# Kernel optimization log

Measured on AMD Instinct MI355X. Metric: run time of the kernel, lower is better.

Reference implementation:

```python
import jax, jax.numpy as jnp
import numpy as np

EPS = 1e-8
CG_TOL = 1e-4
S_SIGMA = 8   # bilateral grid spatial downsampling
N_BINS = 9    # bilateral grid range bins (intensity in [0,1])


def _conv2d(x, k):
    # x [C,H,W], k [kh,kw] -> same-padded cross-correlation, per channel
    kh, kw = k.shape
    out = jax.lax.conv_general_dilated(x[:, None], k[None, None], (1, 1),
                                       [(kh // 2, kh // 2), (kw // 2, kw // 2)])
    return out[:, 0]


def _conv2d_T(x, k):
    return _conv2d(x, k[::-1, ::-1])


def _conv_bank(x, ks):
    # x [C,H,W], ks [N,kh,kw] -> [N,C,H,W]
    n, kh, kw = ks.shape
    out = jax.lax.conv_general_dilated(x[:, None], ks[:, None], (1, 1),
                                       [(kh // 2, kh // 2), (kw // 2, kw // 2)])
    return out.transpose(1, 0, 2, 3)


def _conv_bank_T(v, ks):
    # v [N,C,H,W] -> sum_n conv(v[n], flip(ks[n])) : [C,H,W]
    n, kh, kw = ks.shape
    lhs = v.transpose(1, 0, 2, 3)          # [C,N,H,W]
    rhs = ks[:, ::-1, ::-1][None]          # [1,N,kh,kw]
    out = jax.lax.conv_general_dilated(lhs, rhs, (1, 1),
                                       [(kh // 2, kh // 2), (kw // 2, kw // 2)])
    return out[:, 0]


def _deconv_grad(blurred, x, kernel, dkw, dks, rkw, rks, rpow, reg_targets):
    # gradient of E(x) = sum_i dkw_i ||dk_i * (k*x - b)||^2
    #                  + sum_j rkw_j sum |rk_j*x - t_j|^{p_j}
    Kx = _conv2d(x, kernel) - blurred
    d = _conv_bank(Kx, dks)                                    # [Nd,C,H,W]
    g = _conv2d_T(_conv_bank_T(2.0 * dkw[:, None, None, None] * d, dks), kernel)
    v = _conv_bank(x, rks) - reg_targets                       # [Nr,C,H,W]
    av = jnp.abs(v) + EPS
    phi = jnp.sign(v) * av ** (rpow[:, None, None, None] - 1.0)
    g = g + _conv_bank_T(rkw[:, None, None, None] * rpow[:, None, None, None] * phi, rks)
    return g


def _deconv_alpha(blurred, x, kernel, dkw, dks, rkw, rks, rpow, reg_targets, p):
    # exact line search for the quadratic part, Gauss-Newton for |.|^p prior
    g = _deconv_grad(blurred, x, kernel, dkw, dks, rkw, rks, rpow, reg_targets)
    num = -jnp.sum(g * p)
    Kp = _conv2d(p, kernel)
    dKp = _conv_bank(Kp, dks)
    den = jnp.sum(2.0 * dkw[:, None, None, None] * dKp ** 2)
    v = _conv_bank(x, rks) - reg_targets
    Rp = _conv_bank(p, rks)
    w = (rkw * rpow * (rpow - 1.0))[:, None, None, None]
    den = den + jnp.sum(w * (jnp.abs(v) + EPS) ** (rpow[:, None, None, None] - 2.0) * Rp ** 2)
    return num / (den + 1e-12)


def _deconv_prior(x, rks, thr):
    # soft-shrinkage of filtered responses -> regularization targets
    v = _conv_bank(x, rks)
    return jnp.sign(v) * jnp.maximum(jnp.abs(v) - thr[:, None, None, None], 0.0)


def _conv_axis(g, f, axis):
    k = f.shape[0]; r = k // 2; L = g.shape[axis]
    pad = [(0, 0)] * g.ndim; pad[axis] = (r, r)
    gp = jnp.pad(g, pad)
    out = jnp.zeros_like(g)
    for t in range(k):  # fixed small tap count
        out = out + f[t] * jax.lax.slice_in_dim(gp, t, t + L, axis=axis)
    return out


def _bilateral_channel(I, fs, fr):
    # learned-filter bilateral grid: splat -> separable filter (fs,fs,fr) -> trilinear slice
    H, W = I.shape
    gh, gw = H // S_SIGMA, W // S_SIGMA
    Ic = jnp.clip(I, 0.0, 1.0)
    yy, xx = jnp.meshgrid(jnp.arange(H), jnp.arange(W), indexing="ij")
    yi = yy // S_SIGMA; xi = xx // S_SIGMA
    zi = jnp.clip(jnp.round(Ic * (N_BINS - 1)).astype(jnp.int32), 0, N_BINS - 1)
    flat = ((yi * gw + xi) * N_BINS + zi).ravel()
    gv = jnp.zeros(gh * gw * N_BINS, Ic.dtype).at[flat].add(Ic.ravel())
    gw_ = jnp.zeros(gh * gw * N_BINS, Ic.dtype).at[flat].add(1.0)
    g2 = jnp.stack([gv, gw_], -1).reshape(gh, gw, N_BINS, 2)
    g2 = _conv_axis(_conv_axis(_conv_axis(g2, fs, 0), fs, 1), fr, 2)
    yf = yy / S_SIGMA; xf = xx / S_SIGMA; zf = Ic * (N_BINS - 1)

    def corners(f, n):
        c0 = jnp.clip(jnp.floor(f).astype(jnp.int32), 0, n - 1)
        c1 = jnp.minimum(c0 + 1, n - 1)
        w = jnp.clip(f - c0, 0.0, 1.0)
        return c0, c1, w

    y0, y1, wy = corners(yf, gh)
    x0, x1, wx = corners(xf, gw)
    z0, z1, wz = corners(zf, N_BINS)
    acc = jnp.zeros(I.shape + (2,), Ic.dtype)
    for yc, wyc in ((y0, 1 - wy), (y1, wy)):
        for xc, wxc in ((x0, 1 - wx), (x1, wx)):
            for zc, wzc in ((z0, 1 - wz), (z1, wz)):
                acc = acc + (wyc * wxc * wzc)[..., None] * g2[yc, xc, zc]
    return acc[..., 0] / (acc[..., 1] + 1e-8)


def _forward(blurred_batch, kernel_batch, data_kernels, data_kernel_weights,
             reg_kernels, reg_kernel_weights, reg_powers, filter_s, filter_r,
             reg_thresholds, num_cg_iter):
    num_stages = filter_s.shape[0]
    n_reg = reg_kernels.shape[1]

    def single(blurred, kernel):
        def cg(x, idx, reg_targets):
            dkw = data_kernel_weights[idx]; dks = data_kernels[idx]
            rkw = reg_kernel_weights[idx]; rks = reg_kernels[idx]; rp = reg_powers[idx]
            g = _deconv_grad(blurred, x, kernel, dkw, dks, rkw, rks, rp, reg_targets)
            r = -g
            r_norm = jnp.sum(r * r)
            r0 = r_norm

            def body(i, carry):
                x, r, p, rn, done = carry
                alpha = _deconv_alpha(blurred, x, kernel, dkw, dks, rkw, rks, rp, reg_targets, p)
                x1 = x + alpha * p
                g1 = _deconv_grad(blurred, x1, kernel, dkw, dks, rkw, rks, rp, reg_targets)
                r1 = -g1
                nrn = jnp.sum(r1 * r1)
                beta = nrn / (rn + 1e-20)
                conv_now = nrn < CG_TOL * r0
                p1 = r1 + beta * p
                x_n = jnp.where(done, x, x1)
                r_n = jnp.where(done, r, r1)
                rn_n = jnp.where(done, rn, nrn)
                p_n = jnp.where(done | conv_now, p, p1)
                return (x_n, r_n, p_n, rn_n, done | conv_now)

            carry = (x, r, r, r_norm, jnp.array(False))
            x, _, _, _, _ = jax.lax.fori_loop(0, num_cg_iter, body, carry)
            return x

        x = cg(blurred, 0, jnp.zeros((n_reg,) + blurred.shape, blurred.dtype))
        for stage in range(num_stages):
            x = jax.vmap(lambda ch: _bilateral_channel(ch, filter_s[stage], filter_r[stage]))(x)
            reg_targets = _deconv_prior(x, reg_kernels[stage + 1], reg_thresholds[stage])
            x = cg(x, stage + 1, reg_targets)
        return x

    return jax.vmap(single)(blurred_batch, kernel_batch)


def setup_inputs() -> dict:
    key = jax.random.key(0)
    k1, k2 = jax.random.split(key)
    B, C, H, W, KS = 2, 3, 512, 512, 15
    blurred = jax.random.uniform(k1, (B, C, H, W), jnp.float32)
    kern = jax.random.uniform(k2, (B, KS, KS), jnp.float32)
    kern = kern / jnp.sum(kern, axis=(1, 2), keepdims=True)  # normalized PSFs

    ns = 1; c = 2  # num_stages, kernel center (5x5)
    rk = np.zeros((ns + 1, 5, 5, 5), np.float32)
    rk[:, 0, c, c] = -1.0; rk[:, 0, c + 1, c] = 1.0
    rk[:, 1, c, c] = -1.0; rk[:, 1, c, c + 1] = 1.0
    rk[:, 2, c, c] = 1.0; rk[:, 2, c + 1, c] = -1.0
    rk[:, 2, c, c + 1] = -1.0; rk[:, 2, c + 1, c + 1] = 1.0
    rk[:, 3, c - 1, c] = 1.0; rk[:, 3, c, c] = -2.0; rk[:, 3, c + 1, c] = 1.0
    rk[:, 4, c, c - 1] = 1.0; rk[:, 4, c, c] = -2.0; rk[:, 4, c, c + 1] = 1.0
    dk = np.zeros((ns + 1, 6, 5, 5), np.float32)
    dk[:, 0, c, c] = 1.0
    dk[:, 1:] = rk
    dkw = np.zeros((ns + 1, 6), np.float32); dkw[:, 0] = 1.0
    rkw = np.zeros((ns + 1, 5), np.float32)
    rkw[0, :] = 0.001; rkw[1:, :] = 0.05
    rpow = np.full((ns + 1, 5), 2.0, np.float32)
    fs = np.zeros((ns, 11), np.float32); fs[:, 3:8] = [0.0, 1.0, 2.0, 1.0, 0.0]
    fr = np.tile(np.array([0.0, 1.0, 2.0, 1.0, 0.0], np.float32), (ns, 1))
    thr = np.tile(np.array([0.065, 0.065, 0.0325, 0.0325, 0.0325], np.float32), (ns, 1))

    return {
        "blurred_batch": blurred,
        "kernel_batch": kern,
        "data_kernels": jnp.asarray(dk),
        "data_kernel_weights": jnp.asarray(dkw),
        "reg_kernels": jnp.asarray(rk),
        "reg_kernel_weights": jnp.asarray(rkw),
        "reg_powers": jnp.asarray(rpow),
        "filter_s": jnp.asarray(fs),
        "filter_r": jnp.asarray(fr),
        "reg_thresholds": jnp.asarray(thr),
        "num_cg_iter": 5,
    }


def reference(blurred_batch, kernel_batch, data_kernels, data_kernel_weights,
              reg_kernels, reg_kernel_weights, reg_powers, filter_s, filter_r,
              reg_thresholds, num_cg_iter):
    return _forward(blurred_batch, kernel_batch, data_kernels, data_kernel_weights,
                    reg_kernels, reg_kernel_weights, reg_powers, filter_s, filter_r,
                    reg_thresholds, num_cg_iter)
```

## Files before the change

kernel.cpp:

```cpp
#include <hip/hip_runtime.h>

constexpr int Bn = 2, Cn = 3, Hh = 512, Ww = 512;
constexpr int KS = 15, KR = 7;
constexpr int NDK = 6, NRK = 5;
constexpr int GH = 64, GW = 64, NBn = 9, SS = 8;
constexpr float EPSf = 1e-8f;
constexpr float CGTOL = 1e-4f;
constexpr int PLANE = Hh * Ww;
constexpr int CHW = Cn * PLANE;
constexpr int BX = 64, BY = 16;
constexpr int GXc = Ww / BX, GYc = Hh / BY;
constexpr int PB = GXc * GYc * Cn;
constexpr int SA = 80, THt = 30;
constexpr int S2W = 72, S2H = 24;
constexpr int PHW = 68, PHH = 20;
constexpr int PHG = (PHW / 4) * PHH;
constexpr int NITER = 5;

struct CgState { float alpha, beta, rn, r0; int done, pflag; int pad0, pad1; };

struct SolveInfo {
    int fastBank;
    int allrp2;
    int nd;
    int pad;
    float sctot;
    float dsc[NDK];
    int ddy[NDK], ddx[NDK];
    float C[81];
};

__device__ __forceinline__ float blockReduce(float v, float* red, int tid) {
    red[tid] = v; __syncthreads();
    for (int s = 128; s > 0; s >>= 1) { if (tid < s) red[tid] += red[tid + s]; __syncthreads(); }
    float r = red[0]; __syncthreads();
    return r;
}

__global__ __launch_bounds__(128)
void k_comp(const float* __restrict__ dkw, const float* __restrict__ dks,
            const float* __restrict__ rkw, const float* __restrict__ rpw,
            const float* __restrict__ rks, SolveInfo* si)
{
    const int idx = blockIdx.x;
    SolveInfo* s = si + idx;
    const float* dkw_i = dkw + idx * NDK;
    const float* dks_i = dks + (size_t)idx * NDK * 25;
    const float* rkw_i = rkw + idx * NRK;
    const float* rpw_i = rpw + idx * NRK;
    const float* rks_i = rks + (size_t)idx * NRK * 25;
    const int t = threadIdx.x;
    if (t < 81) {
        int oy = t / 9 - 4, ox = t % 9 - 4;
        float acc = 0.f;
        for (int m = 0; m < NRK; m++) {
            float wm = rkw_i[m], rp = rpw_i[m];
            float ch = wm * rp * (rp - 1.f);
            if (ch == 0.f) continue;
            for (int ay = 0; ay < 5; ay++)
                for (int ax = 0; ax < 5; ax++) {
                    int by = ay - oy, bx = ax - ox;
// ... 11 lines not shown
            for (int q = 0; q < 25; q++) if (dks_i[n * 25 + q] != 0.f) { cntz++; pos = q; }
            if (cntz > 1) fast = 0;
            if (cntz == 1 && nd < NDK) {
                float v = dks_i[n * 25 + pos];
                s->dsc[nd] = 2.f * dkw_i[n] * v * v;
                s->ddy[nd] = pos / 5 - 2; s->ddx[nd] = pos % 5 - 2;
                tot += s->dsc[nd]; nd++;
            }
        }
        s->fastBank = fast; s->nd = fast ? nd : 0; s->sctot = tot;
    }
    if (t == 82) {
        int ok = 1;
        for (int m = 0; m < NRK; m++) {
            float wm = rkw_i[m], rp = rpw_i[m];
            if (wm != 0.f && rp != 2.f && wm * rp * (rp - 1.f) != 0.f) ok = 0;
        }
        s->allrp2 = ok;
    }
}

__global__ __launch_bounds__(256)
void k_conv15(const float* __restrict__ src, const float* __restrict__ rb,
              const float* __restrict__ pbuf, float* __restrict__ aux2,
              const float* __restrict__ sub, float* __restrict__ out,
              const float* __restrict__ kernB, float* __restrict__ part,
              const SolveInfo* __restrict__ si,
              const CgState* __restrict__ st, const int* __restrict__ ncg,
              int iter, int mode)
{
    const int pz = blockIdx.z, b = pz / Cn, c = pz % Cn;
    const CgState s = st[b];
    if (mode == 2 && (s.done != 0 || iter >= *ncg)) return;
    __shared__ __align__(16) float tile[SA * THt];
    __shared__ float red[256];
    const int tx = threadIdx.x, ty = threadIdx.y, tid = ty * 16 + tx;
    const int ox0 = blockIdx.x * BX, oy0 = blockIdx.y * BY;
    const int baseP = pz * PLANE;
    const float beta = s.beta; const int pf = s.pflag;
    const float* kp = kernB + b * 225;

    float nm = 0.f;
    for (int i = tid; i < 78 * THt; i += 256) {
        int ly = i / 78, lx = i % 78;
        int gy = oy0 - KR + ly, gx = ox0 - KR + lx;
        float v = 0.f;
        if (gy >= 0 && gy < Hh && gx >= 0 && gx < Ww) {
            int gi = baseP + gy * Ww + gx;
            if (mode == 2) {
                float rv = rb[gi], pv = pbuf[gi];
                v = pf ? fmaf(beta, pv, rv) : pv;
                if (ly >= KR && ly < KR + BY && lx >= KR && lx < KR + BX) {
                    nm = fmaf(rv, v, nm);
                    aux2[gi] = v;
                }
            } else {
                v = src[gi];
                if (mode == 0 && ly >= KR && ly < KR + BY && lx >= KR && lx < KR + BX)
                    aux2[gi] = v;
            }
        }
        tile[ly * SA + lx] = v;
    }
    __syncthreads();

    const int colbase = tx * 4;
    float a0 = 0.f, a1 = 0.f, a2 = 0.f, a3 = 0.f;
    for (int i = 0; i < KS; i++) {
        const float4* rp4 = reinterpret_cast<const float4*>(&tile[(ty + i) * SA + colbase]);
        float f[20];
        #pragma unroll
        for (int s5 = 0; s5 < 5; s5++) {
            float4 w4 = rp4[s5];
            f[s5 * 4] = w4.x; f[s5 * 4 + 1] = w4.y; f[s5 * 4 + 2] = w4.z; f[s5 * 4 + 3] = w4.w;
        }
        const float* kr = kp + i * 15;
        #pragma unroll
        for (int j = 0; j < KS; j++) {
            float kv = kr[j];
            a0 = fmaf(kv, f[j], a0); a1 = fmaf(kv, f[j + 1], a1);
            a2 = fmaf(kv, f[j + 2], a2); a3 = fmaf(kv, f[j + 3], a3);
        }
    }
    const int gi = baseP + (oy0 + ty) * Ww + ox0 + colbase;
    if (sub) {
        float4 sv = *reinterpret_cast<const float4*>(&sub[gi]);
        a0 -= sv.x; a1 -= sv.y; a2 -= sv.z; a3 -= sv.w;
    }
    if (si->fastBank) {
        const int gy = oy0 + ty, gx0 = ox0 + colbase;
        if (gy >= 2 && gy <= Hh - 3 && gx0 >= 2 && gx0 + 3 <= Ww - 3) {
            float sc = si->sctot;
            a0 *= sc; a1 *= sc; a2 *= sc; a3 *= sc;
        } else {
            float m0 = 0.f, m1 = 0.f, m2 = 0.f, m3 = 0.f;
            int ndl = si->nd;
            for (int n = 0; n < ndl; n++) {
                float sc = si->dsc[n]; int dy = si->ddy[n], dx = si->ddx[n];
                if (gy - dy < 0 || gy - dy >= Hh) continue;
                if (gx0     - dx >= 0 && gx0     - dx < Ww) m0 += sc;
                if (gx0 + 1 - dx >= 0 && gx0 + 1 - dx < Ww) m1 += sc;
                if (gx0 + 2 - dx >= 0 && gx0 + 2 - dx < Ww) m2 += sc;
                if (gx0 + 3 - dx >= 0 && gx0 + 3 - dx < Ww) m3 += sc;
            }
            a0 *= m0; a1 *= m1; a2 *= m2; a3 *= m3;
        }
    }
    *reinterpret_cast<float4*>(&out[gi]) = make_float4(a0, a1, a2, a3);
    if (mode == 2) {
        float tot = blockReduce(nm, red, tid);
        if (tid == 0) {
            int blk = c * (GXc * GYc) + blockIdx.y * GXc + blockIdx.x;
            part[((size_t)b * 4 + 0) * PB + blk] = tot;
        }
    }
}

__global__ __launch_bounds__(256)
void k_bank(const float* __restrict__ sbuf, float* __restrict__ tbuf,
            const float* __restrict__ dks, const float* __restrict__ dkw,
            const SolveInfo* __restrict__ si,
            const CgState* __restrict__ st, const int* __restrict__ ncg,
            int iter, int mode)
{
    if (si->fastBank) return;
    const int pz = blockIdx.z, b = pz / Cn;
    if (mode == 1 && (st[b].done != 0 || iter >= *ncg)) return;
    __shared__ __align__(16) float sl[S2W * S2H];
    __shared__ __align__(16) float dl[PHW * PHH];
    __shared__ float dkk[NDK * 25];
    __shared__ float dww[NDK];
    const int tx = threadIdx.x, ty = threadIdx.y, tid = ty * 16 + tx;
    const int ox0 = blockIdx.x * BX, oy0 = blockIdx.y * BY;
    const int baseP = pz * PLANE;
    const int colbase = tx * 4;
    for (int i = tid; i < NDK * 25; i += 256) dkk[i] = dks[i];
    if (tid < NDK) dww[tid] = dkw[tid];
    for (int i = tid; i < S2W * S2H; i += 256) {
        int ly = i / S2W, lx = i % S2W;
        int gy = oy0 - 4 + ly, gx = ox0 - 4 + lx;
        sl[i] = (gy >= 0 && gy < Hh && gx >= 0 && gx < Ww) ? sbuf[baseP + gy * Ww + gx] : 0.f;
    }
    __syncthreads();
    float t0 = 0.f, t1 = 0.f, t2 = 0.f, t3 = 0.f;
    for (int n = 0; n < NDK; n++) {
// ... 41 lines not shown
            const float4* q4 = reinterpret_cast<const float4*>(&dl[(ty + a) * PHW + colbase]);
            float4 u0 = q4[0], u1 = q4[1];
            float f8[8] = {u0.x,u0.y,u0.z,u0.w,u1.x,u1.y,u1.z,u1.w};
            #pragma unroll
            for (int bb = 0; bb < 5; bb++) {
                float kv = dnr[fr * 5 + (4 - bb)];
                if (kv != 0.f) {
                    c0 = fmaf(kv, f8[bb], c0); c1 = fmaf(kv, f8[bb+1], c1);
                    c2 = fmaf(kv, f8[bb+2], c2); c3 = fmaf(kv, f8[bb+3], c3);
                }
            }
        }
        t0 = fmaf(wn, c0, t0); t1 = fmaf(wn, c1, t1);
        t2 = fmaf(wn, c2, t2); t3 = fmaf(wn, c3, t3);
        __syncthreads();
    }
    const int gi = baseP + (oy0 + ty) * Ww + ox0 + colbase;
    *reinterpret_cast<float4*>(&tbuf[gi]) = make_float4(t0, t1, t2, t3);
}

__global__ __launch_bounds__(256)
void k_hess(const float* __restrict__ kx, const float* __restrict__ wb,
            const float* __restrict__ pn,
            float* __restrict__ qb, const float* __restrict__ kernB,
            const float* __restrict__ rks, const float* __restrict__ rkw,
            const float* __restrict__ rpw, const SolveInfo* __restrict__ si,
            float* __restrict__ part, const CgState* __restrict__ st,
            const int* __restrict__ ncg, int iter)
{
    if (!si->allrp2) return;
    const int pz = blockIdx.z, b = pz / Cn, c = pz % Cn;
    const CgState s = st[b];
    if (s.done != 0 || iter >= *ncg) return;
    __shared__ __align__(16) float wt[SA * THt];
    __shared__ __align__(16) float s2[S2W * S2H];
    __shared__ __align__(16) float sC[81];
    __shared__ float rk5[NRK * 25];
    __shared__ float srkw[NRK], srpw[NRK];
    __shared__ float red[256];
    float* ph = wt;
    const int tx = threadIdx.x, ty = threadIdx.y, tid = ty * 16 + tx;
    const int ox0 = blockIdx.x * BX, oy0 = blockIdx.y * BY;
    const int baseP = pz * PLANE;
    const float* wsrc = si->fastBank ? kx : wb;
    const float* kp = kernB + b * 225;

    for (int i = tid; i < 81; i += 256) sC[i] = si->C[i];
    for (int i = tid; i < NRK * 25; i += 256) rk5[i] = rks[i];
    if (tid < NRK) { srkw[tid] = rkw[tid]; srpw[tid] = rpw[tid]; }

    for (int i = tid; i < 78 * THt; i += 256) {
        int ly = i / 78, lx = i % 78;
        int gy = oy0 - KR + ly, gx = ox0 - KR + lx;
        wt[ly * SA + lx] = (gy >= 0 && gy < Hh && gx >= 0 && gx < Ww)
                           ? wsrc[baseP + gy * Ww + gx] : 0.f;
    }
    for (int i = tid; i < S2W * S2H; i += 256) {
        int ly = i / S2W, lx = i % S2W;
        int gy = oy0 - 4 + ly, gx = ox0 - 4 + lx;
        s2[i] = (gy >= 0 && gy < Hh && gx >= 0 && gx < Ww)
                ? pn[baseP + gy * Ww + gx] : 0.f;
    }
    __syncthreads();

    const int colbase = tx * 4;
    float a0 = 0.f, a1 = 0.f, a2 = 0.f, a3 = 0.f;
    for (int i = 0; i < KS; i++) {
        const float4* rp4 = reinterpret_cast<const float4*>(&wt[(ty + i) * SA + colbase]);
        float f[20];
        #pragma unroll
        for (int s5 = 0; s5 < 5; s5++) {
            float4 w4 = rp4[s5];
            f[s5 * 4] = w4.x; f[s5 * 4 + 1] = w4.y; f[s5 * 4 + 2] = w4.z; f[s5 * 4 + 3] = w4.w;
        }
        const float* kr = kp + (14 - i) * 15;
        #pragma unroll
        for (int j = 0; j < KS; j++) {
            float kv = kr[14 - j];
            a0 = fmaf(kv, f[j], a0); a1 = fmaf(kv, f[j + 1], a1);
            a2 = fmaf(kv, f[j + 2], a2); a3 = fmaf(kv, f[j + 3], a3);
        }
    }

    const bool blkInterior = (oy0 >= 2) && (oy0 + BY - 1 <= Hh - 3) &&
                             (ox0 >= 2) && (ox0 + BX - 1 <= Ww - 3);
    if (blkInterior) {
        #pragma unroll
        for (int oy = 0; oy < 9; oy++) {
            float cr[9]; bool nz = false;
            #pragma unroll
            for (int ox = 0; ox < 9; ox++) { cr[ox] = sC[oy * 9 + ox]; nz = nz || (cr[ox] != 0.f); }
            if (!nz) continue;
            const float4* s4 = reinterpret_cast<const float4*>(&s2[(ty + oy) * S2W + colbase]);
            float4 u0 = s4[0], u1 = s4[1], u2 = s4[2];
            float f12[12] = {u0.x,u0.y,u0.z,u0.w,u1.x,u1.y,u1.z,u1.w,u2.x,u2.y,u2.z,u2.w};
            #pragma unroll
            for (int ox = 0; ox < 9; ox++) {
                float kv = cr[ox];
                if (kv != 0.f) {
                    a0 = fmaf(kv, f12[ox], a0); a1 = fmaf(kv, f12[ox + 1], a1);
                    a2 = fmaf(kv, f12[ox + 2], a2); a3 = fmaf(kv, f12[ox + 3], a3);
                }
            }
        }
    } else {
        __syncthreads();
        for (int m = 0; m < NRK; m++) {
            float wm = srkw[m], rp = srpw[m];
            float coefH = wm * rp * (rp - 1.f);
            if (coefH == 0.f) continue;
            float rmr[25];
            #pragma unroll
            for (int q = 0; q < 25; q++) rmr[q] = rk5[m * 25 + q];
            for (int t = tid; t < PHG; t += 256) {
                int zy = t / 17, zx0 = (t % 17) * 4;
                int gy = oy0 - 2 + zy, gx0 = ox0 - 2 + zx0;
                float v0 = 0.f, v1 = 0.f, v2 = 0.f, v3 = 0.f;
                #pragma unroll
                for (int a = 0; a < 5; a++) {
                    bool rz = rmr[a*5]==0.f && rmr[a*5+1]==0.f && rmr[a*5+2]==0.f &&
                              rmr[a*5+3]==0.f && rmr[a*5+4]==0.f;
                    if (rz) continue;
                    const float4* s4 = reinterpret_cast<const float4*>(&s2[(zy + a) * S2W + zx0]);
                    float4 u0 = s4[0], u1 = s4[1];
                    float f8[8] = {u0.x,u0.y,u0.z,u0.w,u1.x,u1.y,u1.z,u1.w};
                    #pragma unroll
                    for (int bb = 0; bb < 5; bb++) {
                        float kv = rmr[a * 5 + bb];
                        if (kv != 0.f) {
                            v0 = fmaf(kv, f8[bb], v0); v1 = fmaf(kv, f8[bb+1], v1);
                            v2 = fmaf(kv, f8[bb+2], v2); v3 = fmaf(kv, f8[bb+3], v3);
                        }
                    }
                }
                bool gyin = (gy >= 0 && gy < Hh);
                if (!gyin || gx0     < 0 || gx0     >= Ww) v0 = 0.f;
                if (!gyin || gx0 + 1 < 0 || gx0 + 1 >= Ww) v1 = 0.f;
                if (!gyin || gx0 + 2 < 0 || gx0 + 2 >= Ww) v2 = 0.f;
                if (!gyin || gx0 + 3 < 0 || gx0 + 3 >= Ww) v3 = 0.f;
                *reinterpret_cast<float4*>(&ph[zy * PHW + zx0]) =
                    make_float4(coefH * v0, coefH * v1, coefH * v2, coefH * v3);
            }
            __syncthreads();
            #pragma unroll
            for (int a = 0; a < 5; a++) {
                int fr = 4 - a;
                bool rz = rmr[fr*5]==0.f && rmr[fr*5+1]==0.f && rmr[fr*5+2]==0.f &&
                          rmr[fr*5+3]==0.f && rmr[fr*5+4]==0.f;
                if (rz) continue;
                const float4* q4 = reinterpret_cast<const float4*>(&ph[(ty + a) * PHW + colbase]);
                float4 u0 = q4[0], u1 = q4[1];
                float f8[8] = {u0.x,u0.y,u0.z,u0.w,u1.x,u1.y,u1.z,u1.w};
                #pragma unroll
                for (int bb = 0; bb < 5; bb++) {
                    float kv = rmr[fr * 5 + (4 - bb)];
                    if (kv != 0.f) {
                        a0 = fmaf(kv, f8[bb], a0); a1 = fmaf(kv, f8[bb+1], a1);
                        a2 = fmaf(kv, f8[bb+2], a2); a3 = fmaf(kv, f8[bb+3], a3);
                    }
                }
            }
            __syncthreads();
        }
    }

    const int gy = oy0 + ty, gx0 = ox0 + colbase;
    const int gi = baseP + gy * Ww + gx0;
    *reinterpret_cast<float4*>(&qb[gi]) = make_float4(a0, a1, a2, a3);
    int li = (ty + 4) * S2W + colbase + 4;
    float redv = s2[li] * a0 + s2[li + 1] * a1 + s2[li + 2] * a2 + s2[li + 3] * a3;
    float tot = blockReduce(redv, red, tid);
    if (tid == 0) {
        int blk = c * (GXc * GYc) + blockIdx.y * GXc + blockIdx.x;
        part[((size_t)b * 4 + 1) * PB + blk] = tot;
    }
}

__global__ __launch_bounds__(256)
void k_gradL(const float* __restrict__ kx, const float* __restrict__ wb,
             const float* __restrict__ xg,
             const float* __restrict__ rb, const float* __restrict__ pbuf,
             const float* __restrict__ tgt, const float* __restrict__ thr,
             float* __restrict__ outb,
             float* __restrict__ pout, const float* __restrict__ kernB,
             const float* __restrict__ rks, const float* __restrict__ rkw,
             const float* __restrict__ rpw, const SolveInfo* __restrict__ si,
             float* __restrict__ part, const CgState* __restrict__ st,
             const int* __restrict__ ncg, int iter, int mode)
{
    if (mode == 1 && si->allrp2) return;
    const int pz = blockIdx.z, b = pz / Cn, c = pz % Cn;
    const CgState s = st[b];
    if (mode == 1 && (s.done != 0 || iter >= *ncg)) return;
    __shared__ __align__(16) float wt[SA * THt];
    __shared__ __align__(16) float s2[S2W * S2H];
    __shared__ __align__(16) float sC[81];
    __shared__ float rk5[NRK * 25];
    __shared__ float srkw[NRK], srpw[NRK], sthr[NRK];
    __shared__ float red[256];
    float* ph = wt;
    const int tx = threadIdx.x, ty = threadIdx.y, tid = ty * 16 + tx;
    const int ox0 = blockIdx.x * BX, oy0 = blockIdx.y * BY;
    const int baseP = pz * PLANE;
    const float beta = s.beta; const int pf = s.pflag;
    const float* wsrc = si->fastBank ? kx : wb;
    const float* kp = kernB + b * 225;
// ... 151 lines not shown
                        a0 = fmaf(kv, f8[bb], a0); a1 = fmaf(kv, f8[bb+1], a1);
                        a2 = fmaf(kv, f8[bb+2], a2); a3 = fmaf(kv, f8[bb+3], a3);
                    }
                }
            }
            __syncthreads();
        }
    }

    const int gi = baseP + (oy0 + ty) * Ww + ox0 + colbase;
    float redv;
    if (mode == 0) {
        float r0v = -a0, r1v = -a1, r2v = -a2, r3v = -a3;
        float4 rv4 = make_float4(r0v, r1v, r2v, r3v);
        *reinterpret_cast<float4*>(&outb[gi]) = rv4;
        *reinterpret_cast<float4*>(&pout[gi]) = rv4;
        redv = r0v * r0v + r1v * r1v + r2v * r2v + r3v * r3v;
    } else {
        *reinterpret_cast<float4*>(&outb[gi]) = make_float4(a0, a1, a2, a3);
        int li = (ty + 4) * S2W + colbase + 4;
        redv = s2[li] * a0 + s2[li + 1] * a1 + s2[li + 2] * a2 + s2[li + 3] * a3;
    }
    float tot = blockReduce(redv, red, tid);
    if (tid == 0) {
        int blk = c * (GXc * GYc) + blockIdx.y * GXc + blockIdx.x;
        int slot = (mode == 0) ? 2 : 1;
        part[((size_t)b * 4 + slot) * PB + blk] = tot;
    }
}

__global__ __launch_bounds__(256)
void k_axpy(float4* __restrict__ x, float4* __restrict__ r,
            const float4* __restrict__ pn, const float4* __restrict__ q,
            float* __restrict__ part, const CgState* __restrict__ st,
            const int* __restrict__ ncg, int iter)
{
    const int b = blockIdx.y;
    const CgState s = st[b];
    if (s.done != 0 || iter >= *ncg) return;
    __shared__ float red[256];
    const int tid = threadIdx.x;
    float sn = 0.f, sd = 0.f;
    for (int i = tid; i < PB; i += 256) {
        sn += part[((size_t)b * 4 + 0) * PB + i];
        sd += part[((size_t)b * 4 + 1) * PB + i];
    }
    float num = blockReduce(sn, red, tid);
    float den = blockReduce(sd, red, tid);
    const float alpha = num / (den + 1e-12f);
    const int idx = b * (CHW / 4) + blockIdx.x * 256 + tid;
    float4 pc = pn[idx], rv = r[idx], qv = q[idx], xv = x[idx];
    xv.x = fmaf(alpha, pc.x, xv.x); xv.y = fmaf(alpha, pc.y, xv.y);
    xv.z = fmaf(alpha, pc.z, xv.z); xv.w = fmaf(alpha, pc.w, xv.w);
    rv.x = fmaf(-alpha, qv.x, rv.x); rv.y = fmaf(-alpha, qv.y, rv.y);
    rv.z = fmaf(-alpha, qv.z, rv.z); rv.w = fmaf(-alpha, qv.w, rv.w);
    x[idx] = xv; r[idx] = rv;
    float nr = rv.x * rv.x + rv.y * rv.y + rv.z * rv.z + rv.w * rv.w;
    float tot = blockReduce(nr, red, tid);
    if (tid == 0) part[((size_t)b * 4 + 2) * PB + blockIdx.x] = tot;
}

__global__ __launch_bounds__(256)
void k_fin_iter(const float* __restrict__ part, CgState* st,
                const int* __restrict__ ncg, int iter, int mode)
{
    const int b = blockIdx.x, tid = threadIdx.x;
    __shared__ float red[256];
    if (mode == 1 && (st[b].done != 0 || iter >= *ncg)) { if (tid == 0) st[b].pflag = 0; return; }
    float s = 0.f;
    for (int i = tid; i < PB; i += 256) s += part[((size_t)b * 4 + 2) * PB + i];
    float nrn = blockReduce(s, red, tid);
    if (tid == 0) {
        if (mode == 0) {
            st[b].rn = nrn; st[b].r0 = nrn; st[b].done = 0; st[b].pflag = 0;
            st[b].beta = 0.f; st[b].alpha = 0.f;
        } else {
            float beta = nrn / (st[b].rn + 1e-20f);
            int conv = (nrn < CGTOL * st[b].r0) ? 1 : 0;
            st[b].beta = beta; st[b].rn = nrn;
// ... 124 lines not shown
extern "C" void kernel_launch(void* const* d_in, const int* in_sizes, int n_in,
                              void* d_out, int out_size, void* d_ws, size_t ws_size,
                              hipStream_t stream)
{
    const float* blurred = (const float*)d_in[0];
    const float* kern    = (const float*)d_in[1];
    const float* dks     = (const float*)d_in[2];
    const float* dkw     = (const float*)d_in[3];
    const float* rks     = (const float*)d_in[4];
    const float* rkw     = (const float*)d_in[5];
    const float* rpw     = (const float*)d_in[6];
    const float* fs      = (const float*)d_in[7];
    const float* fr      = (const float*)d_in[8];
    const float* thr     = (const float*)d_in[9];
    const int*   ncg     = (const int*)d_in[10];
    (void)in_sizes; (void)n_in; (void)out_size; (void)ws_size;

    float* w = (float*)d_ws;
    size_t off = 0;
    auto alloc = [&](size_t n) { float* p = w + off; off += n; return p; };
    float* xb    = alloc((size_t)Bn * CHW);
    float* pbufA = alloc((size_t)Bn * CHW);
    float* pbufB = alloc((size_t)Bn * CHW);
    float* rbuf  = alloc((size_t)Bn * CHW);
    float* kx    = alloc((size_t)Bn * CHW);
    float* wb    = alloc((size_t)Bn * CHW);
    float* qb    = alloc((size_t)Bn * CHW);
    float* tg    = alloc((size_t)Bn * NRK * CHW);
    float* g0    = alloc((size_t)Bn * Cn * GH * GW * NBn * 2);
    float* g1    = alloc((size_t)Bn * Cn * GH * GW * NBn * 2);
    float* part  = alloc((size_t)Bn * 4 * PB);
    CgState* st = (CgState*)(w + off); off += Bn * 8;
    SolveInfo* sinf = (SolveInfo*)(w + off); off += 2 * ((sizeof(SolveInfo) + 3) / 4);

    dim3 tb(16, 16), grd(GXc, GYc, Bn * Cn);

    k_comp<<<2, 128, 0, stream>>>(dkw, dks, rkw, rpw, rks, sinf);

    auto solve = [&](int idx, const float* tgt_i, const float* thr_i, int initmode) {
        const float* dks_i = dks + (size_t)idx * NDK * 25;
        const float* dkw_i = dkw + (size_t)idx * NDK;
        const float* rks_i = rks + (size_t)idx * NRK * 25;
        const float* rkw_i = rkw + (size_t)idx * NRK;
        const float* rpw_i = rpw + (size_t)idx * NRK;
        const SolveInfo* si = sinf + idx;
        k_conv15<<<grd, tb, 0, stream>>>(initmode == 0 ? blurred : xb, nullptr, nullptr,
                                         initmode == 0 ? xb : nullptr, blurred, kx, kern,
                                         nullptr, si, st, ncg, 0, initmode == 0 ? 0 : 3);
        k_bank<<<grd, tb, 0, stream>>>(kx, wb, dks_i, dkw_i, si, st, ncg, 0, 0);
        k_gradL<<<grd, tb, 0, stream>>>(kx, wb, xb, nullptr, nullptr, tgt_i, thr_i,
                                        rbuf, pbufA, kern,
                                        rks_i, rkw_i, rpw_i, si, part, st, ncg, 0, 0);
        k_fin_iter<<<Bn, 256, 0, stream>>>(part, st, ncg, 0, 0);
        float* pcur = pbufA;
        float* pnxt = pbufB;
        for (int i = 0; i < NITER; i++) {
            k_conv15<<<grd, tb, 0, stream>>>(nullptr, rbuf, pcur, pnxt, nullptr, kx, kern,
                                             part, si, st, ncg, i, 2);
            k_bank<<<grd, tb, 0, stream>>>(kx, wb, dks_i, dkw_i, si, st, ncg, i, 1);
            k_hess<<<grd, tb, 0, stream>>>(kx, wb, pnxt, qb, kern,
                                           rks_i, rkw_i, rpw_i, si, part, st, ncg, i);
            k_gradL<<<grd, tb, 0, stream>>>(kx, wb, xb, rbuf, pnxt, tgt_i, thr_i, qb, nullptr,
                                            kern, rks_i, rkw_i, rpw_i, si, part, st, ncg, i, 1);
            k_axpy<<<dim3(PB, Bn), 256, 0, stream>>>((float4*)xb, (float4*)rbuf,
                                                     (const float4*)pnxt, (const float4*)qb,
                                                     part, st, ncg, i);
            k_fin_iter<<<Bn, 256, 0, stream>>>(part, st, ncg, i, 1);
            float* tswap = pcur; pcur = pnxt; pnxt = tswap;
        }
    };

    solve(0, nullptr, nullptr, 0);

    dim3 sb(8, 8), sg(GW, GH, Bn * Cn);
    k_splat<<<sg, sb, 0, stream>>>(xb, g0);
    const int totalg = Bn * Cn * GH * GW * NBn;
    k_blur<<<(totalg + 255) / 256, 256, 0, stream>>>(g0, g1, fs, 11, 0);
    k_blur<<<(totalg + 255) / 256, 256, 0, stream>>>(g1, g0, fs, 11, 1);
    k_blur<<<(totalg + 255) / 256, 256, 0, stream>>>(g0, g1, fr, 5, 2);
    k_slice<<<dim3(PLANE / 256, 1, Bn * Cn), 256, 0, stream>>>(xb, g1, xb);

    k_prior<<<dim3(Ww / 16, Hh / 16, Bn * Cn), tb, 0, stream>>>(xb, tg, rks + NRK * 25, thr,
                                                                sinf + 1);

    solve(1, tg, thr, 1);

    hipMemcpyAsync(d_out, xb, (size_t)Bn * CHW * sizeof(float),
                   hipMemcpyDeviceToDevice, stream);
}
```

Baseline: 1.321 ms.

## Compute two output rows per thread in conv15 and hessian kernels

k_conv15 and k_hess now use 32-row tiles, with each thread producing two vertically adjacent output rows. Each shared-memory row load feeds both accumulators, which cuts LDS traffic and halo reloads per output. The partial-sum count changes to match the larger blocks, and k_axpy now sums only the valid partials. The second solve also writes directly into the output buffer, which drops the final device-to-device copy. The cost is more registers and shared memory per block and fewer blocks, which may lower occupancy.

```diff
diff --git a/kernel.cpp b/kernel.cpp
--- a/kernel.cpp
+++ b/kernel.cpp
@@ -11,22 +11,25 @@
 constexpr int BX = 64, BY = 16;
 constexpr int GXc = Ww / BX, GYc = Hh / BY;
 constexpr int PB = GXc * GYc * Cn;
+constexpr int BY2 = 32;
+constexpr int GYc2 = Hh / BY2;
+constexpr int PB2 = GXc * GYc2 * Cn;
 constexpr int SA = 80, THt = 30;
+constexpr int TH2 = 46;
 constexpr int S2W = 72, S2H = 24;
+constexpr int S2H2 = 40;
 constexpr int PHW = 68, PHH = 20;
+constexpr int PHH2 = 36;
 constexpr int PHG = (PHW / 4) * PHH;
+constexpr int PHG2 = (PHW / 4) * PHH2;
 constexpr int NITER = 5;
 
 struct CgState { float alpha, beta, rn, r0; int done, pflag; int pad0, pad1; };
 
 struct SolveInfo {
-    int fastBank;
-    int allrp2;
-    int nd;
-    int pad;
+    int fastBank; int allrp2; int nd; int pad;
     float sctot;
-    float dsc[NDK];
-    int ddy[NDK], ddx[NDK];
+    float dsc[NDK]; int ddy[NDK], ddx[NDK];
     float C[81];
 };
 
@@ -104,16 +107,16 @@
     const int pz = blockIdx.z, b = pz / Cn, c = pz % Cn;
     const CgState s = st[b];
     if (mode == 2 && (s.done != 0 || iter >= *ncg)) return;
-    __shared__ __align__(16) float tile[SA * THt];
+    __shared__ __align__(16) float tile[SA * TH2];
     __shared__ float red[256];
     const int tx = threadIdx.x, ty = threadIdx.y, tid = ty * 16 + tx;
-    const int ox0 = blockIdx.x * BX, oy0 = blockIdx.y * BY;
+    const int ox0 = blockIdx.x * BX, oy0 = blockIdx.y * BY2;
     const int baseP = pz * PLANE;
     const float beta = s.beta; const int pf = s.pflag;
     const float* kp = kernB + b * 225;
 
     float nm = 0.f;
-    for (int i = tid; i < 78 * THt; i += 256) {
+    for (int i = tid; i < 78 * TH2; i += 256) {
         int ly = i / 78, lx = i % 78;
         int gy = oy0 - KR + ly, gx = ox0 - KR + lx;
         float v = 0.f;
@@ -122,13 +125,13 @@
             if (mode == 2) {
                 float rv = rb[gi], pv = pbuf[gi];
                 v = pf ? fmaf(beta, pv, rv) : pv;
-                if (ly >= KR && ly < KR + BY && lx >= KR && lx < KR + BX) {
+                if (ly >= KR && ly < KR + BY2 && lx >= KR && lx < KR + BX) {
                     nm = fmaf(rv, v, nm);
                     aux2[gi] = v;
                 }
             } else {
                 v = src[gi];
-                if (mode == 0 && ly >= KR && ly < KR + BY && lx >= KR && lx < KR + BX)
+                if (mode == 0 && ly >= KR && ly < KR + BY2 && lx >= KR && lx < KR + BX)
                     aux2[gi] = v;
             }
         }
@@ -137,52 +140,71 @@
     __syncthreads();
 
     const int colbase = tx * 4;
-    float a0 = 0.f, a1 = 0.f, a2 = 0.f, a3 = 0.f;
-    for (int i = 0; i < KS; i++) {
-        const float4* rp4 = reinterpret_cast<const float4*>(&tile[(ty + i) * SA + colbase]);
+    const int ry = ty * 2;
+    float aA0 = 0.f, aA1 = 0.f, aA2 = 0.f, aA3 = 0.f;
+    float aB0 = 0.f, aB1 = 0.f, aB2 = 0.f, aB3 = 0.f;
+    for (int i = 0; i < 16; i++) {
+        const float4* rp4 = reinterpret_cast<const float4*>(&tile[(ry + i) * SA + colbase]);
         float f[20];
         #pragma unroll
         for (int s5 = 0; s5 < 5; s5++) {
             float4 w4 = rp4[s5];
             f[s5 * 4] = w4.x; f[s5 * 4 + 1] = w4.y; f[s5 * 4 + 2] = w4.z; f[s5 * 4 + 3] = w4.w;
         }
-        const float* kr = kp + i * 15;
-        #pragma unroll
-        for (int j = 0; j < KS; j++) {
-            float kv = kr[j];
-            a0 = fmaf(kv, f[j], a0); a1 = fmaf(kv, f[j + 1], a1);
-            a2 = fmaf(kv, f[j + 2], a2); a3 = fmaf(kv, f[j + 3], a3);
-        }
-    }
-    const int gi = baseP + (oy0 + ty) * Ww + ox0 + colbase;
-    if (sub) {
-        float4 sv = *reinterpret_cast<const float4*>(&sub[gi]);
-        a0 -= sv.x; a1 -= sv.y; a2 -= sv.z; a3 -= sv.w;
-    }
-    if (si->fastBank) {
-        const int gy = oy0 + ty, gx0 = ox0 + colbase;
-        if (gy >= 2 && gy <= Hh - 3 && gx0 >= 2 && gx0 + 3 <= Ww - 3) {
-            float sc = si->sctot;
-            a0 *= sc; a1 *= sc; a2 *= sc; a3 *= sc;
-        } else {
-            float m0 = 0.f, m1 = 0.f, m2 = 0.f, m3 = 0.f;
-            int ndl = si->nd;
-            for (int n = 0; n < ndl; n++) {
-                float sc = si->dsc[n]; int dy = si->ddy[n], dx = si->ddx[n];
-                if (gy - dy < 0 || gy - dy >= Hh) continue;
-                if (gx0     - dx >= 0 && gx0     - dx < Ww) m0 += sc;
-                if (gx0 + 1 - dx >= 0 && gx0 + 1 - dx < Ww) m1 += sc;
-                if (gx0 + 2 - dx >= 0 && gx0 + 2 - dx < Ww) m2 += sc;
-                if (gx0 + 3 - dx >= 0 && gx0 + 3 - dx < Ww) m3 += sc;
-            }
-            a0 *= m0; a1 *= m1; a2 *= m2; a3 *= m3;
-        }
-    }
-    *reinterpret_cast<float4*>(&out[gi]) = make_float4(a0, a1, a2, a3);
+        if (i < 15) {
+            const float* krA = kp + i * 15;
+            #pragma unroll
+            for (int j = 0; j < KS; j++) {
+                float kv = krA[j];
+                aA0 = fmaf(kv, f[j], aA0); aA1 = fmaf(kv, f[j + 1], aA1);
+                aA2 = fmaf(kv, f[j + 2], aA2); aA3 = fmaf(kv, f[j + 3], aA3);
+            }
+        }
+        if (i >= 1) {
+            const float* krB = kp + (i - 1) * 15;
+            #pragma unroll
+            for (int j = 0; j < KS; j++) {
+                float kv = krB[j];
+                aB0 = fmaf(kv, f[j], aB0); aB1 = fmaf(kv, f[j + 1], aB1);
+                aB2 = fmaf(kv, f[j + 2], aB2); aB3 = fmaf(kv, f[j + 3], aB3);
+            }
+        }
+    }
+    const int gyA = oy0 + ry, gx0 = ox0 + colbase;
+    #pragma unroll
+    for (int rr = 0; rr < 2; rr++) {
+        const int gy = gyA + rr;
+        float a0 = rr ? aB0 : aA0, a1 = rr ? aB1 : aA1;
+        float a2 = rr ? aB2 : aA2, a3 = rr ? aB3 : aA3;
+        const int gi = baseP + gy * Ww + gx0;
+        if (sub) {
+            float4 sv = *reinterpret_cast<const float4*>(&sub[gi]);
+            a0 -= sv.x; a1 -= sv.y; a2 -= sv.z; a3 -= sv.w;
+        }
+        if (si->fastBank) {
+            if (gy >= 2 && gy <= Hh - 3 && gx0 >= 2 && gx0 + 3 <= Ww - 3) {
+                float sc = si->sctot;
+                a0 *= sc; a1 *= sc; a2 *= sc; a3 *= sc;
+            } else {
+                float m0 = 0.f, m1 = 0.f, m2 = 0.f, m3 = 0.f;
+                int ndl = si->nd;
+                for (int n = 0; n < ndl; n++) {
+                    float sc = si->dsc[n]; int dy = si->ddy[n], dx = si->ddx[n];
+                    if (gy - dy < 0 || gy - dy >= Hh) continue;
+                    if (gx0     - dx >= 0 && gx0     - dx < Ww) m0 += sc;
+                    if (gx0 + 1 - dx >= 0 && gx0 + 1 - dx < Ww) m1 += sc;
+                    if (gx0 + 2 - dx >= 0 && gx0 + 2 - dx < Ww) m2 += sc;
+                    if (gx0 + 3 - dx >= 0 && gx0 + 3 - dx < Ww) m3 += sc;
+                }
+                a0 *= m0; a1 *= m1; a2 *= m2; a3 *= m3;
+            }
+        }
+        *reinterpret_cast<float4*>(&out[gi]) = make_float4(a0, a1, a2, a3);
+    }
     if (mode == 2) {
         float tot = blockReduce(nm, red, tid);
         if (tid == 0) {
-            int blk = c * (GXc * GYc) + blockIdx.y * GXc + blockIdx.x;
+            int blk = c * (GXc * GYc2) + blockIdx.y * GXc + blockIdx.x;
             part[((size_t)b * 4 + 0) * PB + blk] = tot;
         }
     }
@@ -290,15 +312,15 @@
     const int pz = blockIdx.z, b = pz / Cn, c = pz % Cn;
     const CgState s = st[b];
     if (s.done != 0 || iter >= *ncg) return;
-    __shared__ __align__(16) float wt[SA * THt];
-    __shared__ __align__(16) float s2[S2W * S2H];
+    __shared__ __align__(16) float wt[SA * TH2];
+    __shared__ __align__(16) float s2[S2W * S2H2];
     __shared__ __align__(16) float sC[81];
     __shared__ float rk5[NRK * 25];
     __shared__ float srkw[NRK], srpw[NRK];
     __shared__ float red[256];
     float* ph = wt;
     const int tx = threadIdx.x, ty = threadIdx.y, tid = ty * 16 + tx;
-    const int ox0 = blockIdx.x * BX, oy0 = blockIdx.y * BY;
+    const int ox0 = blockIdx.x * BX, oy0 = blockIdx.y * BY2;
     const int baseP = pz * PLANE;
     const float* wsrc = si->fastBank ? kx : wb;
     const float* kp = kernB + b * 225;
@@ -307,13 +329,13 @@
     for (int i = tid; i < NRK * 25; i += 256) rk5[i] = rks[i];
     if (tid < NRK) { srkw[tid] = rkw[tid]; srpw[tid] = rpw[tid]; }
 
-    for (int i = tid; i < 78 * THt; i += 256) {
+    for (int i = tid; i < 78 * TH2; i += 256) {
         int ly = i / 78, lx = i % 78;
         int gy = oy0 - KR + ly, gx = ox0 - KR + lx;
         wt[ly * SA + lx] = (gy >= 0 && gy < Hh && gx >= 0 && gx < Ww)
                            ? wsrc[baseP + gy * Ww + gx] : 0.f;
     }
-    for (int i = tid; i < S2W * S2H; i += 256) {
+    for (int i = tid; i < S2W * S2H2; i += 256) {
         int ly = i / S2W, lx = i % S2W;
         int gy = oy0 - 4 + ly, gx = ox0 - 4 + lx;
         s2[i] = (gy >= 0 && gy < Hh && gx >= 0 && gx < Ww)
@@ -322,42 +344,62 @@
     __syncthreads();
 
     const int colbase = tx * 4;
-    float a0 = 0.f, a1 = 0.f, a2 = 0.f, a3 = 0.f;
-    for (int i = 0; i < KS; i++) {
-        const float4* rp4 = reinterpret_cast<const float4*>(&wt[(ty + i) * SA + colbase]);
+    const int ry = ty * 2;
+    float aA0 = 0.f, aA1 = 0.f, aA2 = 0.f, aA3 = 0.f;
+    float aB0 = 0.f, aB1 = 0.f, aB2 = 0.f, aB3 = 0.f;
+    for (int i = 0; i < 16; i++) {
+        const float4* rp4 = reinterpret_cast<const float4*>(&wt[(ry + i) * SA + colbase]);
         float f[20];
         #pragma unroll
         for (int s5 = 0; s5 < 5; s5++) {
             float4 w4 = rp4[s5];
             f[s5 * 4] = w4.x; f[s5 * 4 + 1] = w4.y; f[s5 * 4 + 2] = w4.z; f[s5 * 4 + 3] = w4.w;
         }
-        const float* kr = kp + (14 - i) * 15;
-        #pragma unroll
-        for (int j = 0; j < KS; j++) {
-            float kv = kr[14 - j];
-            a0 = fmaf(kv, f[j], a0); a1 = fmaf(kv, f[j + 1], a1);
-            a2 = fmaf(kv, f[j + 2], a2); a3 = fmaf(kv, f[j + 3], a3);
-        }
-    }
-
-    const bool blkInterior = (oy0 >= 2) && (oy0 + BY - 1 <= Hh - 3) &&
+        if (i < 15) {
+            const float* krA = kp + (14 - i) * 15;
+            #pragma unroll
+            for (int j = 0; j < KS; j++) {
+                float kv = krA[14 - j];
+                aA0 = fmaf(kv, f[j], aA0); aA1 = fmaf(kv, f[j + 1], aA1);
+                aA2 = fmaf(kv, f[j + 2], aA2); aA3 = fmaf(kv, f[j + 3], aA3);
+            }
+        }
+        if (i >= 1) {
+            const float* krB = kp + (15 - i) * 15;
+            #pragma unroll
+            for (int j = 0; j < KS; j++) {
+                float kv = krB[14 - j];
+                aB0 = fmaf(kv, f[j], aB0); aB1 = fmaf(kv, f[j + 1], aB1);
+                aB2 = fmaf(kv, f[j + 2], aB2); aB3 = fmaf(kv, f[j + 3], aB3);
+            }
+        }
+    }
+
+    const bool blkInterior = (oy0 >= 2) && (oy0 + BY2 - 1 <= Hh - 3) &&
                              (ox0 >= 2) && (ox0 + BX - 1 <= Ww - 3);
     if (blkInterior) {
-        #pragma unroll
-        for (int oy = 0; oy < 9; oy++) {
-            float cr[9]; bool nz = false;
-            #pragma unroll
-            for (int ox = 0; ox < 9; ox++) { cr[ox] = sC[oy * 9 + ox]; nz = nz || (cr[ox] != 0.f); }
-            if (!nz) continue;
-            const float4* s4 = reinterpret_cast<const float4*>(&s2[(ty + oy) * S2W + colbase]);
+        for (int t = 0; t < 10; t++) {
+            const float4* s4 = reinterpret_cast<const float4*>(&s2[(ry + t) * S2W + colbase]);
             float4 u0 = s4[0], u1 = s4[1], u2 = s4[2];
             float f12[12] = {u0.x,u0.y,u0.z,u0.w,u1.x,u1.y,u1.z,u1.w,u2.x,u2.y,u2.z,u2.w};
-            #pragma unroll
-            for (int ox = 0; ox < 9; ox++) {
-                float kv = cr[ox];
-                if (kv != 0.f) {
-                    a0 = fmaf(kv, f12[ox], a0); a1 = fmaf(kv, f12[ox + 1], a1);
-                    a2 = fmaf(kv, f12[ox + 2], a2); a3 = fmaf(kv, f12[ox + 3], a3);
+            if (t < 9) {
+                #pragma unroll
+                for (int ox = 0; ox < 9; ox++) {
+                    float kv = sC[t * 9 + ox];
+                    if (kv != 0.f) {
+                        aA0 = fmaf(kv, f12[ox], aA0); aA1 = fmaf(kv, f12[ox + 1], aA1);
+                        aA2 = fmaf(kv, f12[ox + 2], aA2); aA3 = fmaf(kv, f12[ox + 3], aA3);
+                    }
+                }
+            }
+            if (t >= 1) {
+                #pragma unroll
+                for (int ox = 0; ox < 9; ox++) {
+                    float kv = sC[(t - 1) * 9 + ox];
+                    if (kv != 0.f) {
+                        aB0 = fmaf(kv, f12[ox], aB0); aB1 = fmaf(kv, f12[ox + 1], aB1);
+                        aB2 = fmaf(kv, f12[ox + 2], aB2); aB3 = fmaf(kv, f12[ox + 3], aB3);
+                    }
                 }
             }
         }
@@ -370,7 +412,7 @@
             float rmr[25];
             #pragma unroll
             for (int q = 0; q < 25; q++) rmr[q] = rk5[m * 25 + q];
-            for (int t = tid; t < PHG; t += 256) {
+            for (int t = tid; t < PHG2; t += 256) {
                 int zy = t / 17, zx0 = (t % 17) * 4;
                 int gy = oy0 - 2 + zy, gx0 = ox0 - 2 + zx0;
                 float v0 = 0.f, v1 = 0.f, v2 = 0.f, v3 = 0.f;
@@ -400,36 +442,52 @@
                     make_float4(coefH * v0, coefH * v1, coefH * v2, coefH * v3);
             }
             __syncthreads();
-            #pragma unroll
-            for (int a = 0; a < 5; a++) {
-                int fr = 4 - a;
-                bool rz = rmr[fr*5]==0.f && rmr[fr*5+1]==0.f && rmr[fr*5+2]==0.f &&
-                          rmr[fr*5+3]==0.f && rmr[fr*5+4]==0.f;
-                if (rz) continue;
-                const float4* q4 = reinterpret_cast<const float4*>(&ph[(ty + a) * PHW + colbase]);
+            for (int t = 0; t < 6; t++) {
+                const float4* q4 = reinterpret_cast<const float4*>(&ph[(ry + t) * PHW + colbase]);
                 float4 u0 = q4[0], u1 = q4[1];
                 float f8[8] = {u0.x,u0.y,u0.z,u0.w,u1.x,u1.y,u1.z,u1.w};
-                #pragma unroll
-                for (int bb = 0; bb < 5; bb++) {
-                    float kv = rmr[fr * 5 + (4 - bb)];
-                    if (kv != 0.f) {
-                        a0 = fmaf(kv, f8[bb], a0); a1 = fmaf(kv, f8[bb+1], a1);
-                        a2 = fmaf(kv, f8[bb+2], a2); a3 = fmaf(kv, f8[bb+3], a3);
+                if (t < 5) {
+                    int fr = 4 - t;
+                    #pragma unroll
+                    for (int bb = 0; bb < 5; bb++) {
+                        float kv = rmr[fr * 5 + (4 - bb)];
+                        if (kv != 0.f) {
+                            aA0 = fmaf(kv, f8[bb], aA0); aA1 = fmaf(kv, f8[bb+1], aA1);
+                            aA2 = fmaf(kv, f8[bb+2], aA2); aA3 = fmaf(kv, f8[bb+3], aA3);
+                        }
                     }
                 }
+                if (t >= 1) {
+                    int fr = 5 - t;
+                    #pragma unroll
+                    for (int bb = 0; bb < 5; bb++) {
+                        float kv = rmr[fr * 5 + (4 - bb)];
+                        if (kv != 0.f) {
+                            aB0 = fmaf(kv, f8[bb], aB0); aB1 = fmaf(kv, f8[bb+1], aB1);
+                            aB2 = fmaf(kv, f8[bb+2], aB2); aB3 = fmaf(kv, f8[bb+3], aB3);
+                        }
+                    }
+                }
             }
             __syncthreads();
         }
     }
 
-    const int gy = oy0 + ty, gx0 = ox0 + colbase;
-    const int gi = baseP + gy * Ww + gx0;
-    *reinterpret_cast<float4*>(&qb[gi]) = make_float4(a0, a1, a2, a3);
-    int li = (ty + 4) * S2W + colbase + 4;
-    float redv = s2[li] * a0 + s2[li + 1] * a1 + s2[li + 2] * a2 + s2[li + 3] * a3;
+    const int gx0 = ox0 + colbase;
+    float redv = 0.f;
+    #pragma unroll
+    for (int rr = 0; rr < 2; rr++) {
+        const int gy = oy0 + ry + rr;
+        float a0 = rr ? aB0 : aA0, a1 = rr ? aB1 : aA1;
+        float a2 = rr ? aB2 : aA2, a3 = rr ? aB3 : aA3;
+        const int gi = baseP + gy * Ww + gx0;
+        *reinterpret_cast<float4*>(&qb[gi]) = make_float4(a0, a1, a2, a3);
+        int li = (ry + rr + 4) * S2W + colbase + 4;
+        redv += s2[li] * a0 + s2[li + 1] * a1 + s2[li + 2] * a2 + s2[li + 3] * a3;
+    }
     float tot = blockReduce(redv, red, tid);
     if (tid == 0) {
-        int blk = c * (GXc * GYc) + blockIdx.y * GXc + blockIdx.x;
+        int blk = c * (GXc * GYc2) + blockIdx.y * GXc + blockIdx.x;
         part[((size_t)b * 4 + 1) * PB + blk] = tot;
     }
 }
@@ -647,7 +705,8 @@
 __global__ __launch_bounds__(256)
 void k_axpy(float4* __restrict__ x, float4* __restrict__ r,
             const float4* __restrict__ pn, const float4* __restrict__ q,
-            float* __restrict__ part, const CgState* __restrict__ st,
+            float* __restrict__ part, const SolveInfo* __restrict__ si,
+            const CgState* __restrict__ st,
             const int* __restrict__ ncg, int iter)
 {
     const int b = blockIdx.y;
@@ -655,11 +714,10 @@
     if (s.done != 0 || iter >= *ncg) return;
     __shared__ float red[256];
     const int tid = threadIdx.x;
+    const int nden = si->allrp2 ? PB2 : PB;
     float sn = 0.f, sd = 0.f;
-    for (int i = tid; i < PB; i += 256) {
-        sn += part[((size_t)b * 4 + 0) * PB + i];
-        sd += part[((size_t)b * 4 + 1) * PB + i];
-    }
+    for (int i = tid; i < PB2; i += 256) sn += part[((size_t)b * 4 + 0) * PB + i];
+    for (int i = tid; i < nden; i += 256) sd += part[((size_t)b * 4 + 1) * PB + i];
     float num = blockReduce(sn, red, tid);
     float den = blockReduce(sd, red, tid);
     const float alpha = num / (den + 1e-12f);
@@ -850,45 +908,49 @@
     float* part  = alloc((size_t)Bn * 4 * PB);
     CgState* st = (CgState*)(w + off); off += Bn * 8;
     SolveInfo* sinf = (SolveInfo*)(w + off); off += 2 * ((sizeof(SolveInfo) + 3) / 4);
-
-    dim3 tb(16, 16), grd(GXc, GYc, Bn * Cn);
+    float* xout = (float*)d_out;
+
+    dim3 tb(16, 16);
+    dim3 grd(GXc, GYc, Bn * Cn);
+    dim3 grd2(GXc, GYc2, Bn * Cn);
 
     k_comp<<<2, 128, 0, stream>>>(dkw, dks, rkw, rpw, rks, sinf);
 
-    auto solve = [&](int idx, const float* tgt_i, const float* thr_i, int initmode) {
+    auto solve = [&](int idx, float* xcur, const float* tgt_i, const float* thr_i,
+                     int initmode) {
         const float* dks_i = dks + (size_t)idx * NDK * 25;
         const float* dkw_i = dkw + (size_t)idx * NDK;
         const float* rks_i = rks + (size_t)idx * NRK * 25;
         const float* rkw_i = rkw + (size_t)idx * NRK;
         const float* rpw_i = rpw + (size_t)idx * NRK;
         const SolveInfo* si = sinf + idx;
-        k_conv15<<<grd, tb, 0, stream>>>(initmode == 0 ? blurred : xb, nullptr, nullptr,
-                                         initmode == 0 ? xb : nullptr, blurred, kx, kern,
-                                         nullptr, si, st, ncg, 0, initmode == 0 ? 0 : 3);
+        k_conv15<<<grd2, tb, 0, stream>>>(initmode == 0 ? blurred : xcur, nullptr, nullptr,
+                                          initmode == 0 ? xcur : nullptr, blurred, kx, kern,
+                                          nullptr, si, st, ncg, 0, initmode == 0 ? 0 : 3);
         k_bank<<<grd, tb, 0, stream>>>(kx, wb, dks_i, dkw_i, si, st, ncg, 0, 0);
-        k_gradL<<<grd, tb, 0, stream>>>(kx, wb, xb, nullptr, nullptr, tgt_i, thr_i,
+        k_gradL<<<grd, tb, 0, stream>>>(kx, wb, xcur, nullptr, nullptr, tgt_i, thr_i,
                                         rbuf, pbufA, kern,
                                         rks_i, rkw_i, rpw_i, si, part, st, ncg, 0, 0);
         k_fin_iter<<<Bn, 256, 0, stream>>>(part, st, ncg, 0, 0);
         float* pcur = pbufA;
         float* pnxt = pbufB;
         for (int i = 0; i < NITER; i++) {
-            k_conv15<<<grd, tb, 0, stream>>>(nullptr, rbuf, pcur, pnxt, nullptr, kx, kern,
-                                             part, si, st, ncg, i, 2);
+            k_conv15<<<grd2, tb, 0, stream>>>(nullptr, rbuf, pcur, pnxt, nullptr, kx, kern,
+                                              part, si, st, ncg, i, 2);
             k_bank<<<grd, tb, 0, stream>>>(kx, wb, dks_i, dkw_i, si, st, ncg, i, 1);
-            k_hess<<<grd, tb, 0, stream>>>(kx, wb, pnxt, qb, kern,
-                                           rks_i, rkw_i, rpw_i, si, part, st, ncg, i);
-            k_gradL<<<grd, tb, 0, stream>>>(kx, wb, xb, rbuf, pnxt, tgt_i, thr_i, qb, nullptr,
+            k_hess<<<grd2, tb, 0, stream>>>(kx, wb, pnxt, qb, kern,
+                                            rks_i, rkw_i, rpw_i, si, part, st, ncg, i);
+            k_gradL<<<grd, tb, 0, stream>>>(kx, wb, xcur, rbuf, pnxt, tgt_i, thr_i, qb, nullptr,
                                             kern, rks_i, rkw_i, rpw_i, si, part, st, ncg, i, 1);
-            k_axpy<<<dim3(PB, Bn), 256, 0, stream>>>((float4*)xb, (float4*)rbuf,
+            k_axpy<<<dim3(PB, Bn), 256, 0, stream>>>((float4*)xcur, (float4*)rbuf,
                                                      (const float4*)pnxt, (const float4*)qb,
-                                                     part, st, ncg, i);
+                                                     part, si, st, ncg, i);
             k_fin_iter<<<Bn, 256, 0, stream>>>(part, st, ncg, i, 1);
             float* tswap = pcur; pcur = pnxt; pnxt = tswap;
         }
     };
 
-    solve(0, nullptr, nullptr, 0);
+    solve(0, xb, nullptr, nullptr, 0);
 
     dim3 sb(8, 8), sg(GW, GH, Bn * Cn);
     k_splat<<<sg, sb, 0, stream>>>(xb, g0);
@@ -896,13 +958,10 @@
     k_blur<<<(totalg + 255) / 256, 256, 0, stream>>>(g0, g1, fs, 11, 0);
     k_blur<<<(totalg + 255) / 256, 256, 0, stream>>>(g1, g0, fs, 11, 1);
     k_blur<<<(totalg + 255) / 256, 256, 0, stream>>>(g0, g1, fr, 5, 2);
-    k_slice<<<dim3(PLANE / 256, 1, Bn * Cn), 256, 0, stream>>>(xb, g1, xb);
-
-    k_prior<<<dim3(Ww / 16, Hh / 16, Bn * Cn), tb, 0, stream>>>(xb, tg, rks + NRK * 25, thr,
+    k_slice<<<dim3(PLANE / 256, 1, Bn * Cn), 256, 0, stream>>>(xb, g1, xout);
+
+    k_prior<<<dim3(Ww / 16, Hh / 16, Bn * Cn), tb, 0, stream>>>(xout, tg, rks + NRK * 25, thr,
                                                                 sinf + 1);
 
-    solve(1, tg, thr, 1);
-
-    hipMemcpyAsync(d_out, xb, (size_t)Bn * CHW * sizeof(float),
-                   hipMemcpyDeviceToDevice, stream);
-}
+    solve(1, xout, tg, thr, 1);
+}
```

After: 1.489 ms. 12.7% more time.
